# Kernel tuning notes

Measured on AMD Instinct MI355X. Metric: run time of the kernel, lower is better.

The kernel has to match this reference:

```python
import jax, jax.numpy as jnp
import numpy as np

N_NODES = 50000
N_REL = 10
N_TRIPLES = 500000
BATCH = 16384
HIDDEN = 64
OUT = 64


def setup_inputs() -> dict:
    key = jax.random.key(0)
    ks = jax.random.split(key, 10)
    n, r, E, B = N_NODES, N_REL, N_TRIPLES, BATCH
    r2 = 2 * r + 1
    s = jax.random.randint(ks[0], (E,), 0, n)
    p = jax.random.randint(ks[1], (E,), 0, r)
    o = jax.random.randint(ks[2], (E,), 0, n)
    triples = jnp.stack([s, p, o], axis=1)
    bs = jax.random.randint(ks[3], (B,), 0, n)
    bp = jax.random.randint(ks[4], (B,), 0, r)
    bo = jax.random.randint(ks[5], (B,), 0, n)
    batch = jnp.stack([bs, bp, bo], axis=1)
    # xavier_uniform w/ relu gain: bound = sqrt(2)*sqrt(6/(fan_in+fan_out))
    g = np.sqrt(2.0)
    bound0 = g * np.sqrt(6.0 / (n * HIDDEN + r2 * HIDDEN))
    w0 = jax.random.uniform(ks[6], (r2, n, HIDDEN), minval=-bound0, maxval=bound0, dtype=jnp.float32)
    bound1 = g * np.sqrt(6.0 / (HIDDEN * OUT + r2 * OUT))
    w1 = jax.random.uniform(ks[7], (r2, HIDDEN, OUT), minval=-bound1, maxval=bound1, dtype=jnp.float32)
    b0 = jnp.zeros((HIDDEN,), jnp.float32)
    b1 = jnp.zeros((OUT,), jnp.float32)
    relations = jax.random.uniform(ks[8], (r, OUT), minval=-0.85, maxval=0.85, dtype=jnp.float32)
    return {"batch": batch, "triples": triples, "w0": w0, "b0": b0,
            "w1": w1, "b1": b1, "relations": relations}


def _rgcn_forward(triples, w0, b0, w1, b1, n, r):
    """Two-layer horizontal RGCN: layer0 featureless, layer1 dense input."""
    r2 = 2 * r + 1
    s, p, o = triples[:, 0], triples[:, 1], triples[:, 2]
    ar = jnp.arange(n, dtype=s.dtype)
    # add_inverse_and_self: [triples ; self-loops (rel 2r) ; inverses (rel p+r)]
    s_all = jnp.concatenate([s, ar, o])
    p_all = jnp.concatenate([p, jnp.full((n,), 2 * r, dtype=p.dtype), p + r])
    o_all = jnp.concatenate([o, ar, s])
    col = p_all * n + o_all              # horizontal adj column index in (n, r2*n)
    e = s_all.shape[0]
    vals = jnp.ones((e,), jnp.float32)
    # normalize by column sums (sum_sparse with row=False for hor=True)
    colsum = jax.ops.segment_sum(vals, col, num_segments=r2 * n)
    vals = vals / colsum[col]
    # layer0: out = adj @ w0.reshape(r2*n, hidden); row s sums vals * w0[p, o]
    w0f = w0.reshape(r2 * n, -1)
    h = jax.ops.segment_sum(vals[:, None] * w0f[col], s_all, num_segments=n) + b0
    # layer1: nw[r, n] = h[n] @ w1[r]; out row s sums vals * nw[p, o]
    nw = jnp.einsum('ni,rio->rno', h, w1).reshape(r2 * n, -1)
    nodes = jax.ops.segment_sum(vals[:, None] * nw[col], s_all, num_segments=n) + b1
    return nodes


def reference(batch, triples, w0, b0, w1, b1, relations):
    n = w0.shape[1]
    r = relations.shape[0]
    nodes = _rgcn_forward(triples, w0, b0, w1, b1, n, r)
    si, pi, oi = batch[:, 0], batch[:, 1], batch[:, 2]
    # distmult score: sum_d s_d * p_d * o_d
    scores = jnp.sum(nodes[si] * relations[pi] * nodes[oi], axis=-1)
    return scores
```

## Files before the change

kernel.cpp:

```cpp
#include <hip/hip_runtime.h>

#define NN 50000
#define NR 10
#define R2 21
#define NE 500000
#define NB 16384
#define HID 64
#define SCAN_B 1024
#define NLX 32768

__global__ void hist_kernel(const int* __restrict__ triples, const int* __restrict__ batch,
                            int* __restrict__ cnt, int* __restrict__ celloff,
                            int* __restrict__ rank, int* __restrict__ flag) {
    int t = blockIdx.x * blockDim.x + threadIdx.x;
    if (t < 2 * NE) {
        int e = (t < NE) ? t : t - NE;
        int s = triples[3 * e], p = triples[3 * e + 1], o = triples[3 * e + 2];
        int ss, dst, src;
        if (t < NE) { ss = p;      dst = s; src = o; }
        else        { ss = p + NR; dst = o; src = s; }
        rank[t] = atomicAdd(celloff + dst * R2 + ss, 1);
        atomicAdd(cnt + ss * NN + src, 1);
    } else if (t < 2 * NE + NN) {
        int v = t - 2 * NE;
        celloff[v * R2 + 2 * NR] = 1;
        cnt[2 * NR * NN + v] = 1;
    } else if (t < 2 * NE + NN + 2 * NB) {
        int j = t - (2 * NE + NN);
        int node = (j < NB) ? batch[3 * j] : batch[3 * (j - NB) + 2];
        flag[node] = 1;
    }
}

__global__ void recip_kernel(int* __restrict__ cnt) {
    int i = blockIdx.x * blockDim.x + threadIdx.x;
    if (i < R2 * NN) {
        int c = cnt[i];
        ((float*)cnt)[i] = 1.0f / (float)c;
    }
}

__global__ void compact_kernel(const int* __restrict__ flag, int* __restrict__ nl_count,
                               int* __restrict__ list, int* __restrict__ inv) {
    int t = blockIdx.x * blockDim.x + threadIdx.x;
    if (t < NN && flag[t]) {
        int s = atomicAdd(nl_count, 1);
        list[s] = t;
        inv[t] = s;
    }
}

__global__ void scan1_kernel(int* __restrict__ data, int* __restrict__ bsums, int M) {
    __shared__ int sm[SCAN_B];
    int i0 = (blockIdx.x * SCAN_B + threadIdx.x) * 2;
    int x0 = (i0     < M) ? data[i0]     : 0;
    int x1 = (i0 + 1 < M) ? data[i0 + 1] : 0;
    int s = x0 + x1;
    sm[threadIdx.x] = s; __syncthreads();
    for (int off = 1; off < SCAN_B; off <<= 1) {
        int v = (threadIdx.x >= off) ? sm[threadIdx.x - off] : 0;
        __syncthreads();
        sm[threadIdx.x] += v;
        __syncthreads();
    }
    int excl = sm[threadIdx.x] - s;
    if (i0     < M) data[i0]     = excl;
    if (i0 + 1 < M) data[i0 + 1] = excl + x0;
    if (threadIdx.x == SCAN_B - 1) bsums[blockIdx.x] = sm[SCAN_B - 1];
}
__global__ void scan2_kernel(int* __restrict__ bsums, int nb, int* __restrict__ total_out) {
    __shared__ int sm[SCAN_B];
    int x = (threadIdx.x < nb) ? bsums[threadIdx.x] : 0;
    sm[threadIdx.x] = x; __syncthreads();
    for (int off = 1; off < SCAN_B; off <<= 1) {
        int v = (threadIdx.x >= off) ? sm[threadIdx.x - off] : 0;
        __syncthreads();
        sm[threadIdx.x] += v;
        __syncthreads();
    }
    if (threadIdx.x < nb) bsums[threadIdx.x] = sm[threadIdx.x] - x;
    if (threadIdx.x == SCAN_B - 1) *total_out = sm[SCAN_B - 1];
}
__global__ void scan3_kernel(int* __restrict__ data, const int* __restrict__ bsums, int M) {
    int i0 = (blockIdx.x * SCAN_B + threadIdx.x) * 2;
    int b = bsums[blockIdx.x];
    if (i0     < M) data[i0]     += b;
    if (i0 + 1 < M) data[i0 + 1] += b;
}

__global__ void scatter_kernel(const int* __restrict__ triples,
                               const int* __restrict__ celloff,
                               const int* __restrict__ rank,
                               int* __restrict__ pay) {
    int t = blockIdx.x * blockDim.x + threadIdx.x;
    if (t >= 2 * NE + NN) return;
    if (t < 2 * NE) {
        int e = (t < NE) ? t : t - NE;
        int s = triples[3 * e], p = triples[3 * e + 1], o = triples[3 * e + 2];
        int ss, dst, src;
        if (t < NE) { ss = p;      dst = s; src = o; }
        else        { ss = p + NR; dst = o; src = s; }
        int pos = celloff[dst * R2 + ss] + rank[t];
        pay[pos] = ss * NN + src;
    } else {
        int v = t - 2 * NE;
        int pos = celloff[v * R2 + 2 * NR];
        pay[pos] = 2 * NR * NN + v;
    }
}

__global__ __launch_bounds__(256) void layer1_kernel(const int* __restrict__ celloff,
                                                     const int* __restrict__ pay,
                                                     const float* __restrict__ vals,
                                                     const float* __restrict__ w0,
                                                     const float* __restrict__ b0,
                                                     float* __restrict__ h) {
    int wv = (blockIdx.x * blockDim.x + threadIdx.x) >> 6;
    int lane = threadIdx.x & 63;
    if (wv >= NN) return;
    int dst = __builtin_amdgcn_readfirstlane(wv);
    int beg = celloff[dst * R2];
    int end = celloff[(dst + 1) * R2];
    float acc = b0[lane];
    for (int base = beg; base < end; base += 64) {
        int idx = base + lane;
        int colv = (idx < end) ? pay[idx] : 2 * NR * NN;
        float vv = (idx < end) ? vals[colv] : 0.f;
        int m = __builtin_amdgcn_readfirstlane(min(64, end - base));
        int e = 0;
        for (; e + 4 <= m; e += 4) {
            int   c0_ = __shfl(colv, e,     64); float v0 = __shfl(vv, e,     64);
            int   c1_ = __shfl(colv, e + 1, 64); float v1 = __shfl(vv, e + 1, 64);
            int   c2_ = __shfl(colv, e + 2, 64); float v2 = __shfl(vv, e + 2, 64);
            int   c3_ = __shfl(colv, e + 3, 64); float v3 = __shfl(vv, e + 3, 64);
            float f0 = w0[(size_t)c0_ * HID + lane];
            float f1 = w0[(size_t)c1_ * HID + lane];
            float f2 = w0[(size_t)c2_ * HID + lane];
            float f3 = w0[(size_t)c3_ * HID + lane];
            acc += v0 * f0; acc += v1 * f1; acc += v2 * f2; acc += v3 * f3;
        }
        for (; e < m; ++e) {
            int   c = __shfl(colv, e, 64);
            float v = __shfl(vv, e, 64);
            acc += v * w0[(size_t)c * HID + lane];
        }
    }
    h[(size_t)dst * HID + lane] = acc;
}

__global__ __launch_bounds__(256) void hc_kernel(const float* __restrict__ h,
                                                 const int* __restrict__ list,
                                                 const int* __restrict__ nl_count,
                                                 float* __restrict__ h_c) {
    int wv = (blockIdx.x * blockDim.x + threadIdx.x) >> 6;
    int lane = threadIdx.x & 63;
    if (wv >= *nl_count) return;
    int node = __builtin_amdgcn_readfirstlane(list[wv]);
    h_c[(size_t)wv * HID + lane] = h[(size_t)node * HID + lane];
}

__global__ __launch_bounds__(256) void phaseA_kernel(const int* __restrict__ celloff,
                                                     const int* __restrict__ pay,
                                                     const float* __restrict__ vals,
                                                     const float* __restrict__ h,
                                                     const int* __restrict__ list,
                                                     const int* __restrict__ nl_count,
                                                     float* __restrict__ agg) {
    int wv = (blockIdx.x * blockDim.x + threadIdx.x) >> 6;
    int lane = threadIdx.x & 63;
    if (wv >= *nl_count) return;
    int i = wv;
    int dst = __builtin_amdgcn_readfirstlane(list[i]);
    int beg = celloff[dst * R2];
    int end = celloff[dst * R2 + 2 * NR];
    float* ab = agg + (size_t)i * HID + lane;
    int cur = 0;
    float a = 0.f;
    for (int e = beg; e < end; ++e) {
        int col = __builtin_amdgcn_readfirstlane(pay[e]);
        int ss = col / NN;
        if (ss != cur) {
            ab[(size_t)cur * NLX * HID] = a;
            for (int r = cur + 1; r < ss; ++r) ab[(size_t)r * NLX * HID] = 0.f;
            a = 0.f; cur = ss;
        }
        int src = col - ss * NN;
        a += vals[col] * h[(size_t)src * HID + lane];
    }
    ab[(size_t)cur * NLX * HID] = a;
    for (int r = cur + 1; r < 2 * NR; ++r) ab[(size_t)r * NLX * HID] = 0.f;
}

__global__ __launch_bounds__(256) void phaseB_kernel(const float* __restrict__ agg,
                                                     const float* __restrict__ h_c,
                                                     const float* __restrict__ w1,
                                                     const int* __restrict__ nl_count,
                                                     float* __restrict__ nodes_c) {
    __shared__ float lds[32 * 68];
    const int nl = *nl_count;
    const int rbase = blockIdx.x * 32;
    if (rbase >= nl) return;
    const int lane = threadIdx.x & 63;
    const int wid = __builtin_amdgcn_readfirstlane(threadIdx.x >> 6);
    const int trow = threadIdx.x >> 3;
    const int tc8 = threadIdx.x & 7;
    const int grow = rbase + trow;

    float acc[8];
#pragma unroll
    for (int i = 0; i < 8; ++i) acc[i] = 0.f;

    for (int r = 0; r <= 2 * NR; ++r) {
        const float* Ab = (r < 2 * NR) ? (agg + (size_t)r * NLX * HID) : h_c;
#pragma unroll
        for (int it = 0; it < 2; ++it) {
            int c = tc8 + 8 * it;
            float4 v = make_float4(0.f, 0.f, 0.f, 0.f);
            if (grow < nl) v = *(const float4*)(Ab + (size_t)grow * HID + c * 4);
            *(float4*)(lds + trow * 68 + c * 4) = v;
        }
        __syncthreads();

        const float* wp = w1 + (size_t)r * HID * HID;
#pragma unroll
        for (int kc = 0; kc < 4; ++kc) {
            float wk[16];
#pragma unroll
            for (int k = 0; k < 16; ++k) wk[k] = wp[(kc * 16 + k) * HID + lane];
#pragma unroll
            for (int ii = 0; ii < 8; ++ii) {
                const float* lp = lds + (wid * 8 + ii) * 68 + kc * 16;
                float4 a0 = *(const float4*)(lp);
                float4 a1 = *(const float4*)(lp + 4);
                float4 a2 = *(const float4*)(lp + 8);
                float4 a3 = *(const float4*)(lp + 12);
                float a = acc[ii];
                a += a0.x * wk[0];  a += a0.y * wk[1];  a += a0.z * wk[2];  a += a0.w * wk[3];
                a += a1.x * wk[4];  a += a1.y * wk[5];  a += a1.z * wk[6];  a += a1.w * wk[7];
                a += a2.x * wk[8];  a += a2.y * wk[9];  a += a2.z * wk[10]; a += a2.w * wk[11];
                a += a3.x * wk[12]; a += a3.y * wk[13]; a += a3.z * wk[14]; a += a3.w * wk[15];
                acc[ii] = a;
            }
        }
        __syncthreads();
    }

#pragma unroll
    for (int ii = 0; ii < 8; ++ii) {
        int i = rbase + wid * 8 + ii;
        if (i < nl) nodes_c[(size_t)i * HID + lane] = acc[ii];
    }
}

__global__ __launch_bounds__(256) void score_kernel(const int* __restrict__ batch,
                                                    const float* __restrict__ nodes_c,
                                                    const int* __restrict__ inv,
                                                    const float* __restrict__ b1,
                                                    const float* __restrict__ rel,
                                                    float* __restrict__ out) {
    int wave = (blockIdx.x * blockDim.x + threadIdx.x) >> 6;
    int lane = threadIdx.x & 63;
    if (wave >= NB) return;
    int si = batch[3 * wave], pi = batch[3 * wave + 1], oi = batch[3 * wave + 2];
    float a = nodes_c[(size_t)inv[si] * HID + lane] + b1[lane];
    float b = nodes_c[(size_t)inv[oi] * HID + lane] + b1[lane];
    float v = a * rel[pi * HID + lane] * b;
#pragma unroll
    for (int off = 32; off; off >>= 1) v += __shfl_down(v, off, 64);
    if (lane == 0) out[wave] = v;
}

extern "C" void kernel_launch(void* const* d_in, const int* in_sizes, int n_in,
                              void* d_out, int out_size, void* d_ws, size_t ws_size,
                              hipStream_t stream) {
    const int*   batch   = (const int*)d_in[0];
    const int*   triples = (const int*)d_in[1];
    const float* w0      = (const float*)d_in[2];
    const float* b0      = (const float*)d_in[3];
    const float* w1      = (const float*)d_in[4];
    const float* b1      = (const float*)d_in[5];
    const float* rel     = (const float*)d_in[6];
    float* out = (float*)d_out;

    int* cnt      = (int*)d_ws;
    int* celloff  = cnt + (size_t)R2 * NN;
    int* flag     = celloff + ((size_t)R2 * NN + 1);
    int* nl_count = flag + NN;
    int* rank     = nl_count + 1;
    int* pay      = rank + 2 * NE;
    int* sums     = pay + (2 * NE + NN);
    int* list     = sums + SCAN_B;
    int* inv      = list + NLX;
    float* h      = (float*)(inv + NN);
    float* h_c    = h + (size_t)NN * HID;
    float* nodes_c= h_c + (size_t)NLX * HID;
    float* agg    = nodes_c + (size_t)NLX * HID;
    const float* vals = (const float*)cnt;

    size_t zero_bytes = ((size_t)2 * R2 * NN + 1 + NN + 1) * 4;
    hipMemsetAsync(d_ws, 0, zero_bytes, stream);

    const int tot = 2 * NE + NN + 2 * NB;
    hist_kernel<<<(tot + 255) / 256, 256, 0, stream>>>(triples, batch, cnt, celloff, rank, flag);
    recip_kernel<<<(R2 * NN + 255) / 256, 256, 0, stream>>>(cnt);
    compact_kernel<<<(NN + 255) / 256, 256, 0, stream>>>(flag, nl_count, list, inv);

    {
        int M = R2 * NN;
        int nb = (M + 2 * SCAN_B - 1) / (2 * SCAN_B);
        scan1_kernel<<<nb, SCAN_B, 0, stream>>>(celloff, sums, M);
        scan2_kernel<<<1, SCAN_B, 0, stream>>>(sums, nb, celloff + M);
        scan3_kernel<<<nb, SCAN_B, 0, stream>>>(celloff, sums, M);
    }

    scatter_kernel<<<(2 * NE + NN + 255) / 256, 256, 0, stream>>>(triples, celloff, rank, pay);

    layer1_kernel<<<(NN * 64 + 255) / 256, 256, 0, stream>>>(celloff, pay, vals, w0, b0, h);

    hc_kernel<<<(NLX * 64) / 256, 256, 0, stream>>>(h, list, nl_count, h_c);

    phaseA_kernel<<<(NLX * 64) / 256, 256, 0, stream>>>(celloff, pay, vals, h, list, nl_count, agg);

    phaseB_kernel<<<NLX / 32, 256, 0, stream>>>(agg, h_c, w1, nl_count, nodes_c);

    score_kernel<<<(NB * 64 + 255) / 256, 256, 0, stream>>>(batch, nodes_c, inv, b1, rel, out);
}
```

Baseline: 701.9 us.

## Derive column counts from cell histogram, fuse h_c gather into layer1, batch phaseA loads

Drops the separate column-count histogram and gets each normalization count from the matching inverse-relation cell count in celloff before the scan runs. This removes one atomic per edge and halves the memset. The hist and scatter kernels now handle both directions of each triple in one thread, and layer1 writes compacted h_c directly, so hc_kernel is gone. Layer1's gather loop is unrolled to 8, and phaseA loads pay and vals cooperatively per 64-edge chunk and broadcasts them with shuffles instead of doing serial scalar loads.

```diff
diff --git a/kernel.cpp b/kernel.cpp
--- a/kernel.cpp
+++ b/kernel.cpp
@@ -10,34 +10,33 @@
 #define NLX 32768
 
 __global__ void hist_kernel(const int* __restrict__ triples, const int* __restrict__ batch,
-                            int* __restrict__ cnt, int* __restrict__ celloff,
-                            int* __restrict__ rank, int* __restrict__ flag) {
+                            int* __restrict__ celloff, int* __restrict__ rank,
+                            int* __restrict__ flag) {
     int t = blockIdx.x * blockDim.x + threadIdx.x;
-    if (t < 2 * NE) {
-        int e = (t < NE) ? t : t - NE;
-        int s = triples[3 * e], p = triples[3 * e + 1], o = triples[3 * e + 2];
-        int ss, dst, src;
-        if (t < NE) { ss = p;      dst = s; src = o; }
-        else        { ss = p + NR; dst = o; src = s; }
-        rank[t] = atomicAdd(celloff + dst * R2 + ss, 1);
-        atomicAdd(cnt + ss * NN + src, 1);
-    } else if (t < 2 * NE + NN) {
-        int v = t - 2 * NE;
+    if (t < NE) {
+        int s = triples[3 * t], p = triples[3 * t + 1], o = triples[3 * t + 2];
+        rank[t]      = atomicAdd(celloff + s * R2 + p, 1);
+        rank[t + NE] = atomicAdd(celloff + o * R2 + (p + NR), 1);
+    } else if (t < NE + NN) {
+        int v = t - NE;
         celloff[v * R2 + 2 * NR] = 1;
-        cnt[2 * NR * NN + v] = 1;
-    } else if (t < 2 * NE + NN + 2 * NB) {
-        int j = t - (2 * NE + NN);
+    } else if (t < NE + NN + 2 * NB) {
+        int j = t - (NE + NN);
         int node = (j < NB) ? batch[3 * j] : batch[3 * (j - NB) + 2];
         flag[node] = 1;
     }
 }
 
-__global__ void recip_kernel(int* __restrict__ cnt) {
+__global__ void recip_kernel(const int* __restrict__ celloff, float* __restrict__ vals) {
     int i = blockIdx.x * blockDim.x + threadIdx.x;
-    if (i < R2 * NN) {
-        int c = cnt[i];
-        ((float*)cnt)[i] = 1.0f / (float)c;
-    }
+    if (i >= R2 * NN) return;
+    unsigned ss = (unsigned)i / NN;
+    int x = i - ss * NN;
+    int c;
+    if (ss < NR)          c = celloff[x * R2 + ss + NR];
+    else if (ss < 2 * NR) c = celloff[x * R2 + ss - NR];
+    else                  c = 1;
+    vals[i] = 1.0f / (float)c;
 }
 
 __global__ void compact_kernel(const int* __restrict__ flag, int* __restrict__ nl_count,
@@ -93,17 +92,14 @@
                                const int* __restrict__ rank,
                                int* __restrict__ pay) {
     int t = blockIdx.x * blockDim.x + threadIdx.x;
-    if (t >= 2 * NE + NN) return;
-    if (t < 2 * NE) {
-        int e = (t < NE) ? t : t - NE;
-        int s = triples[3 * e], p = triples[3 * e + 1], o = triples[3 * e + 2];
-        int ss, dst, src;
-        if (t < NE) { ss = p;      dst = s; src = o; }
-        else        { ss = p + NR; dst = o; src = s; }
-        int pos = celloff[dst * R2 + ss] + rank[t];
-        pay[pos] = ss * NN + src;
-    } else {
-        int v = t - 2 * NE;
+    if (t < NE) {
+        int s = triples[3 * t], p = triples[3 * t + 1], o = triples[3 * t + 2];
+        int pos1 = celloff[s * R2 + p] + rank[t];
+        pay[pos1] = p * NN + o;
+        int pos2 = celloff[o * R2 + (p + NR)] + rank[t + NE];
+        pay[pos2] = (p + NR) * NN + s;
+    } else if (t < NE + NN) {
+        int v = t - NE;
         int pos = celloff[v * R2 + 2 * NR];
         pay[pos] = 2 * NR * NN + v;
     }
@@ -114,7 +110,10 @@
                                                      const float* __restrict__ vals,
                                                      const float* __restrict__ w0,
                                                      const float* __restrict__ b0,
-                                                     float* __restrict__ h) {
+                                                     const int* __restrict__ flag,
+                                                     const int* __restrict__ inv,
+                                                     float* __restrict__ h,
+                                                     float* __restrict__ h_c) {
     int wv = (blockIdx.x * blockDim.x + threadIdx.x) >> 6;
     int lane = threadIdx.x & 63;
     if (wv >= NN) return;
@@ -128,16 +127,25 @@
         float vv = (idx < end) ? vals[colv] : 0.f;
         int m = __builtin_amdgcn_readfirstlane(min(64, end - base));
         int e = 0;
-        for (; e + 4 <= m; e += 4) {
-            int   c0_ = __shfl(colv, e,     64); float v0 = __shfl(vv, e,     64);
-            int   c1_ = __shfl(colv, e + 1, 64); float v1 = __shfl(vv, e + 1, 64);
-            int   c2_ = __shfl(colv, e + 2, 64); float v2 = __shfl(vv, e + 2, 64);
-            int   c3_ = __shfl(colv, e + 3, 64); float v3 = __shfl(vv, e + 3, 64);
+        for (; e + 8 <= m; e += 8) {
+            int c0_ = __shfl(colv, e,     64); float v0 = __shfl(vv, e,     64);
+            int c1_ = __shfl(colv, e + 1, 64); float v1 = __shfl(vv, e + 1, 64);
+            int c2_ = __shfl(colv, e + 2, 64); float v2 = __shfl(vv, e + 2, 64);
+            int c3_ = __shfl(colv, e + 3, 64); float v3 = __shfl(vv, e + 3, 64);
+            int c4_ = __shfl(colv, e + 4, 64); float v4 = __shfl(vv, e + 4, 64);
+            int c5_ = __shfl(colv, e + 5, 64); float v5 = __shfl(vv, e + 5, 64);
+            int c6_ = __shfl(colv, e + 6, 64); float v6 = __shfl(vv, e + 6, 64);
+            int c7_ = __shfl(colv, e + 7, 64); float v7 = __shfl(vv, e + 7, 64);
             float f0 = w0[(size_t)c0_ * HID + lane];
             float f1 = w0[(size_t)c1_ * HID + lane];
             float f2 = w0[(size_t)c2_ * HID + lane];
             float f3 = w0[(size_t)c3_ * HID + lane];
+            float f4 = w0[(size_t)c4_ * HID + lane];
+            float f5 = w0[(size_t)c5_ * HID + lane];
+            float f6 = w0[(size_t)c6_ * HID + lane];
+            float f7 = w0[(size_t)c7_ * HID + lane];
             acc += v0 * f0; acc += v1 * f1; acc += v2 * f2; acc += v3 * f3;
+            acc += v4 * f4; acc += v5 * f5; acc += v6 * f6; acc += v7 * f7;
         }
         for (; e < m; ++e) {
             int   c = __shfl(colv, e, 64);
@@ -146,17 +154,7 @@
         }
     }
     h[(size_t)dst * HID + lane] = acc;
-}
-
-__global__ __launch_bounds__(256) void hc_kernel(const float* __restrict__ h,
-                                                 const int* __restrict__ list,
-                                                 const int* __restrict__ nl_count,
-                                                 float* __restrict__ h_c) {
-    int wv = (blockIdx.x * blockDim.x + threadIdx.x) >> 6;
-    int lane = threadIdx.x & 63;
-    if (wv >= *nl_count) return;
-    int node = __builtin_amdgcn_readfirstlane(list[wv]);
-    h_c[(size_t)wv * HID + lane] = h[(size_t)node * HID + lane];
+    if (flag[dst]) h_c[(size_t)inv[dst] * HID + lane] = acc;
 }
 
 __global__ __launch_bounds__(256) void phaseA_kernel(const int* __restrict__ celloff,
@@ -166,6 +164,7 @@
                                                      const int* __restrict__ list,
                                                      const int* __restrict__ nl_count,
                                                      float* __restrict__ agg) {
+    const size_t SL = (size_t)NLX * HID;
     int wv = (blockIdx.x * blockDim.x + threadIdx.x) >> 6;
     int lane = threadIdx.x & 63;
     if (wv >= *nl_count) return;
@@ -176,19 +175,26 @@
     float* ab = agg + (size_t)i * HID + lane;
     int cur = 0;
     float a = 0.f;
-    for (int e = beg; e < end; ++e) {
-        int col = __builtin_amdgcn_readfirstlane(pay[e]);
-        int ss = col / NN;
-        if (ss != cur) {
-            ab[(size_t)cur * NLX * HID] = a;
-            for (int r = cur + 1; r < ss; ++r) ab[(size_t)r * NLX * HID] = 0.f;
-            a = 0.f; cur = ss;
-        }
-        int src = col - ss * NN;
-        a += vals[col] * h[(size_t)src * HID + lane];
-    }
-    ab[(size_t)cur * NLX * HID] = a;
-    for (int r = cur + 1; r < 2 * NR; ++r) ab[(size_t)r * NLX * HID] = 0.f;
+    for (int base = beg; base < end; base += 64) {
+        int idx = base + lane;
+        int colv = (idx < end) ? pay[idx] : 0;
+        float vv = (idx < end) ? vals[colv] : 0.f;
+        int m = __builtin_amdgcn_readfirstlane(min(64, end - base));
+        for (int e = 0; e < m; ++e) {
+            int   c = __shfl(colv, e, 64);
+            float v = __shfl(vv, e, 64);
+            int ss = (int)((unsigned)c / NN);
+            if (ss != cur) {
+                ab[(size_t)cur * SL] = a;
+                for (int r = cur + 1; r < ss; ++r) ab[(size_t)r * SL] = 0.f;
+                a = 0.f; cur = ss;
+            }
+            int src = c - ss * NN;
+            a += v * h[(size_t)src * HID + lane];
+        }
+    }
+    ab[(size_t)cur * SL] = a;
+    for (int r = cur + 1; r < 2 * NR; ++r) ab[(size_t)r * SL] = 0.f;
 }
 
 __global__ __launch_bounds__(256) void phaseB_kernel(const float* __restrict__ agg,
@@ -282,11 +288,11 @@
     const float* rel     = (const float*)d_in[6];
     float* out = (float*)d_out;
 
-    int* cnt      = (int*)d_ws;
-    int* celloff  = cnt + (size_t)R2 * NN;
+    int* celloff  = (int*)d_ws;
     int* flag     = celloff + ((size_t)R2 * NN + 1);
     int* nl_count = flag + NN;
-    int* rank     = nl_count + 1;
+    float* vals   = (float*)(nl_count + 1);
+    int* rank     = (int*)(vals + (size_t)R2 * NN);
     int* pay      = rank + 2 * NE;
     int* sums     = pay + (2 * NE + NN);
     int* list     = sums + SCAN_B;
@@ -295,14 +301,13 @@
     float* h_c    = h + (size_t)NN * HID;
     float* nodes_c= h_c + (size_t)NLX * HID;
     float* agg    = nodes_c + (size_t)NLX * HID;
-    const float* vals = (const float*)cnt;
-
-    size_t zero_bytes = ((size_t)2 * R2 * NN + 1 + NN + 1) * 4;
+
+    size_t zero_bytes = ((size_t)R2 * NN + 1 + NN + 1) * 4;
     hipMemsetAsync(d_ws, 0, zero_bytes, stream);
 
-    const int tot = 2 * NE + NN + 2 * NB;
-    hist_kernel<<<(tot + 255) / 256, 256, 0, stream>>>(triples, batch, cnt, celloff, rank, flag);
-    recip_kernel<<<(R2 * NN + 255) / 256, 256, 0, stream>>>(cnt);
+    const int htot = NE + NN + 2 * NB;
+    hist_kernel<<<(htot + 255) / 256, 256, 0, stream>>>(triples, batch, celloff, rank, flag);
+    recip_kernel<<<(R2 * NN + 255) / 256, 256, 0, stream>>>(celloff, vals);
     compact_kernel<<<(NN + 255) / 256, 256, 0, stream>>>(flag, nl_count, list, inv);
 
     {
@@ -313,11 +318,10 @@
         scan3_kernel<<<nb, SCAN_B, 0, stream>>>(celloff, sums, M);
     }
 
-    scatter_kernel<<<(2 * NE + NN + 255) / 256, 256, 0, stream>>>(triples, celloff, rank, pay);
-
-    layer1_kernel<<<(NN * 64 + 255) / 256, 256, 0, stream>>>(celloff, pay, vals, w0, b0, h);
-
-    hc_kernel<<<(NLX * 64) / 256, 256, 0, stream>>>(h, list, nl_count, h_c);
+    scatter_kernel<<<(NE + NN + 255) / 256, 256, 0, stream>>>(triples, celloff, rank, pay);
+
+    layer1_kernel<<<(NN * 64 + 255) / 256, 256, 0, stream>>>(celloff, pay, vals, w0, b0,
+                                                             flag, inv, h, h_c);
 
     phaseA_kernel<<<(NLX * 64) / 256, 256, 0, stream>>>(celloff, pay, vals, h, list, nl_count, agg);
 
```

After: 658.1 us. 6.2% less time.
